# Optimization experiments

Measured on AMD Instinct MI355X. Metric: run time of the kernel, lower is better.

## Reference

```python
import jax, jax.numpy as jnp
import numpy as np

DIM = 512; HEADS = 8; DH = 64; INNER = HEADS * DH
GAMMA = 0.01; LREG = 1e-3
QB = 16; NS = 512


def _ln(x, g, b):
    mu = x.mean(-1, keepdims=True)
    var = jnp.var(x, axis=-1, keepdims=True)  # biased, matches torch LayerNorm
    return (x - mu) / jnp.sqrt(var + 1e-5) * g + b


def _std(x):
    return jnp.std(x, ddof=1)  # torch.std default is unbiased


def setup_inputs() -> dict:
    key = jax.random.key(0)
    ks = jax.random.split(key, 10)
    sc = lambda k, shape: (jax.random.normal(k, shape, jnp.float32) * 0.05)
    return {
        "q": jax.random.normal(ks[0], (QB, NS, DIM), jnp.float32),
        "k": jax.random.normal(ks[1], (QB, NS, DIM), jnp.float32),
        "v": jax.random.normal(ks[2], (QB, NS, DIM), jnp.float32),
        "ln1_g": jnp.ones((DIM,), jnp.float32),
        "ln1_b": jnp.zeros((DIM,), jnp.float32),
        "W_in": sc(ks[3], (DIM, INNER)),
        "wp_w1": sc(ks[4], (2 * DH, 2 * DH)),
        "wp_b1": jnp.zeros((2 * DH,), jnp.float32),
        "wp_ln_g": jnp.ones((2 * DH,), jnp.float32),
        "wp_ln_b": jnp.zeros((2 * DH,), jnp.float32),
        "wp_w2": sc(ks[5], (2 * DH, DH)),
        "wp_b2": jnp.zeros((DH,), jnp.float32),
        "wp_w3": sc(ks[6], (DH, 3)),
        "wp_b3": jnp.zeros((3,), jnp.float32),
        "weight_temp": jnp.array([0.5], jnp.float32),
        "W_out": sc(ks[7], (INNER, DIM)),
        "b_out": jnp.zeros((DIM,), jnp.float32),
    }


def _forward(q, k, v, ln1_g, ln1_b, W_in, wp_w1, wp_b1, wp_ln_g, wp_ln_b,
             wp_w2, wp_b2, wp_w3, wp_b3, weight_temp, W_out, b_out):
    eps = 1e-6

    def proj(t):  # LayerNorm -> Linear(no bias) -> [h, q, n, d]
        y = _ln(t, ln1_g, ln1_b) @ W_in
        Qb, Nb, _ = y.shape
        return y.reshape(Qb, Nb, HEADS, DH).transpose(2, 0, 1, 3)

    f_q, f_k, f_v = proj(q), proj(k), proj(v)
    m = f_k.shape[2]

    # --- cosine distance component ---
    dots_raw = jnp.einsum('hqnd,hqmd->hqnm', f_q, f_k)
    n1 = jnp.linalg.norm(f_q, axis=-1, keepdims=True) + eps          # [h,q,n,1]
    n2 = jnp.linalg.norm(f_k, axis=-1)[:, :, None, :] + eps          # [h,q,1,m]
    cosine_sim = jnp.clip(dots_raw / (n1 * n2), -0.9, 0.9)

    # --- regularized covariance component ---
    fkc = f_k - f_k.mean(axis=2, keepdims=True)   # center keys over n
    fqc = f_q - f_q.mean(axis=-1, keepdims=True)  # center queries over d
    cov = jnp.einsum('hqnd,hqmd->hqnm', fqc, fkc) / (DH ** 0.5 + 1e-6)
    cov = jnp.clip((LREG / max(m, 1)) * cov, -10.0, 10.0)

    # --- margin-based variance component (eval: adaptive_gamma = gamma) ---
    fqn = f_q / jnp.maximum(jnp.linalg.norm(f_q, axis=-1, keepdims=True), 1e-6)
    fkn = f_k / jnp.maximum(jnp.linalg.norm(f_k, axis=-1, keepdims=True), 1e-6)
    cs = jnp.clip(jnp.einsum('hqnd,hqmd->hqnm', fqn, fkn), -0.9, 0.9)
    margin = jnp.clip(GAMMA - cs, 0.0, 5.0)
    var_comp = jnp.broadcast_to(margin.mean(-1, keepdims=True), cs.shape)

    # --- dynamic per-head mixture weights ---
    feat = jnp.concatenate([f_q.mean((1, 2)), f_k.mean((1, 2))], axis=-1)  # [h, 2d]
    x = jax.nn.relu(_ln(feat @ wp_w1 + wp_b1, wp_ln_g, wp_ln_b))
    x = jax.nn.relu(x @ wp_w2 + wp_b2)
    wlog = jax.nn.softmax(x @ wp_w3 + wp_b3, axis=-1)  # predictor ends in Softmax
    wt = jnp.clip(weight_temp, 0.1, 2.0)
    w = jax.nn.softmax(wlog / wt, axis=-1)             # second softmax over temp
    w = jnp.clip(w, 0.05, 0.8)
    w = w / w.sum(-1, keepdims=True)
    cos_w = w[:, 0].reshape(HEADS, 1, 1, 1)
    cov_w = w[:, 1].reshape(HEADS, 1, 1, 1)
    var_w = w[:, 2].reshape(HEADS, 1, 1, 1)

    sg = jax.lax.stop_gradient  # norms are .detach()'d in torch
    dots = (cos_w * (cosine_sim / (sg(_std(cosine_sim)) + 1e-6))
            + cov_w * (cov / (sg(_std(cov)) + 1e-6) * 0.5)
            + var_w * (var_comp / (sg(_std(var_comp)) + 1e-6) * 0.5))

    ds = _std(dots)
    temp = jnp.where(ds < 1e-4, jnp.float32(0.1),
                     jnp.where(ds < 0.01, jnp.float32(0.3), 0.5 + ds))
    temp = jnp.clip(temp, 0.1, 3.0)

    attn = jax.nn.softmax(dots / temp, axis=-1)
    out = jnp.einsum('hqnm,hqmd->hqnd', attn, f_v)
    out = out.transpose(1, 2, 0, 3).reshape(q.shape[0], q.shape[1], INNER)
    return out @ W_out + b_out


def reference(q, k, v, ln1_g, ln1_b, W_in, wp_w1, wp_b1, wp_ln_g, wp_ln_b,
              wp_w2, wp_b2, wp_w3, wp_b3, weight_temp, W_out, b_out):
    return _forward(q, k, v, ln1_g, ln1_b, W_in, wp_w1, wp_b1, wp_ln_g,
                    wp_ln_b, wp_w2, wp_b2, wp_w3, wp_b3, weight_temp,
                    W_out, b_out)
```

## Files before the change

kernel.cpp:

```cpp
#include <hip/hip_runtime.h>
#include <math.h>

#define H 8
#define NS 512
#define D 64

typedef __bf16 bf16x8 __attribute__((ext_vector_type(8)));
typedef float f32x4 __attribute__((ext_vector_type(4)));
typedef short s16x8 __attribute__((ext_vector_type(8)));
typedef short s16x4 __attribute__((ext_vector_type(4)));

#define CS2 ((1e-3f/512.f)/(8.f+1e-6f))

static __device__ __forceinline__ f32x4 mfma16(bf16x8 a, bf16x8 b, f32x4 c){
  return __builtin_amdgcn_mfma_f32_16x16x32_bf16(a,b,c,0,0,0);
}
static __device__ __forceinline__ float b2f(unsigned short s){
  union { unsigned u; float f; } v; v.u = ((unsigned)s)<<16; return v.f;
}
static __device__ __forceinline__ unsigned short f2b(float f){
  union { float f; unsigned u; } v; v.f = f;
  unsigned r = v.u + 0x7FFFu + ((v.u>>16)&1u);
  return (unsigned short)(r>>16);
}
static __device__ __forceinline__ float wred64(float v){
  #pragma unroll
  for(int m=32; m>0; m>>=1) v += __shfl_xor(v, m, 64);
  return v;
}

constexpr size_t OFF_XNB = 0;
constexpr size_t OFF_FQB = 6291456;
constexpr size_t OFF_FKB = 8388608;
constexpr size_t OFF_FVB = 10485760;
constexpr size_t OFF_FVT = 12582912;
constexpr size_t OFF_WT  = 14680064;
constexpr size_t OFF_WOH = 14811136;
constexpr size_t OFF_WOL = 14942208;
constexpr size_t OFF_OHH = 15073280;
constexpr size_t OFF_OHL = 17170432;
constexpr size_t OFF_ARR = 19267584;
constexpr size_t OFF_MKB = OFF_ARR + 9*65536;
constexpr size_t OFF_SMK = OFF_MKB + 8192;
constexpr size_t OFF_COEF= OFF_SMK + 128;
constexpr size_t OFF_DBL = OFF_COEF + 32;
constexpr size_t NDBL    = 72 + 1024;

__global__ __launch_bounds__(256) void k_tw(const float* __restrict__ W, unsigned short* __restrict__ WT,
    double* __restrict__ dbl){
  int bx = blockIdx.x; int kt = bx>>3, nt = bx&7;
  int t = threadIdx.x;
  if(bx==0){
    for(int i=t;i<(int)NDBL;i+=256) dbl[i]=0.0;
  }
  __shared__ float tile[64][65];
  #pragma unroll
  for(int i=0;i<4;i++){
    int row = (t>>4) + i*16; int col = (t&15)*4;
    float4 v = *(const float4*)(W + (size_t)(kt*64+row)*512 + nt*64 + col);
    tile[row][col]=v.x; tile[row][col+1]=v.y; tile[row][col+2]=v.z; tile[row][col+3]=v.w;
  }
  __syncthreads();
  #pragma unroll
  for(int i=0;i<4;i++){
    int n = (t>>4) + i*16; int ck = (t&15)*4;
    s16x4 o;
    #pragma unroll
    for(int j=0;j<4;j++) o[j] = (short)f2b(tile[ck+j][n]);
    *(s16x4*)(WT + (size_t)(nt*64+n)*512 + kt*64 + ck) = o;
  }
}

__global__ __launch_bounds__(256) void k_two(const float* __restrict__ W,
    unsigned short* __restrict__ WTh, unsigned short* __restrict__ WTl){
  int bx = blockIdx.x; int kt = bx>>3, nt = bx&7;
  __shared__ float tile[64][65];
  int t = threadIdx.x;
  #pragma unroll
  for(int i=0;i<4;i++){
    int row = (t>>4) + i*16; int col = (t&15)*4;
    float4 v = *(const float4*)(W + (size_t)(kt*64+row)*512 + nt*64 + col);
    tile[row][col]=v.x; tile[row][col+1]=v.y; tile[row][col+2]=v.z; tile[row][col+3]=v.w;
  }
  __syncthreads();
  #pragma unroll
  for(int i=0;i<4;i++){
    int n = (t>>4) + i*16; int ck = (t&15)*4;
    s16x4 oh_, ol_;
    #pragma unroll
    for(int j=0;j<4;j++){
      float x = tile[ck+j][n];
      unsigned short hi = f2b(x);
      oh_[j] = (short)hi;
      ol_[j] = (short)f2b(x - b2f(hi));
    }
    *(s16x4*)(WTh + (size_t)(nt*64+n)*512 + kt*64 + ck) = oh_;
    *(s16x4*)(WTl + (size_t)(nt*64+n)*512 + kt*64 + ck) = ol_;
  }
}

__global__ __launch_bounds__(256) void k_ln(const float* __restrict__ q,
    const float* __restrict__ k, const float* __restrict__ v,
    const float* __restrict__ g, const float* __restrict__ b,
    unsigned short* __restrict__ xnb){
  int row = blockIdx.x*4 + (threadIdx.x>>6); int t = threadIdx.x & 63;
  const float* src = (row < 8192) ? q : ((row < 16384) ? k : v);
  int r = row & 8191;
  const float4* sp = (const float4*)(src + (size_t)r*512);
  float4 v1 = sp[t*2], v2 = sp[t*2+1];
  float s  = v1.x+v1.y+v1.z+v1.w + v2.x+v2.y+v2.z+v2.w;
  float ss = v1.x*v1.x+v1.y*v1.y+v1.z*v1.z+v1.w*v1.w
           + v2.x*v2.x+v2.y*v2.y+v2.z*v2.z+v2.w*v2.w;
  s = wred64(s); ss = wred64(ss);
  float mu = s*(1.f/512.f);
  float var = ss*(1.f/512.f) - mu*mu;
  float rstd = rsqrtf(var + 1e-5f);
  const float4* gp = (const float4*)g; const float4* bp = (const float4*)b;
  float4 g1 = gp[t*2], g2 = gp[t*2+1], b1 = bp[t*2], b2 = bp[t*2+1];
  s16x8 o;
  o[0]=(short)f2b((v1.x-mu)*rstd*g1.x+b1.x); o[1]=(short)f2b((v1.y-mu)*rstd*g1.y+b1.y);
  o[2]=(short)f2b((v1.z-mu)*rstd*g1.z+b1.z); o[3]=(short)f2b((v1.w-mu)*rstd*g1.w+b1.w);
  o[4]=(short)f2b((v2.x-mu)*rstd*g2.x+b2.x); o[5]=(short)f2b((v2.y-mu)*rstd*g2.y+b2.y);
  o[6]=(short)f2b((v2.z-mu)*rstd*g2.z+b2.z); o[7]=(short)f2b((v2.w-mu)*rstd*g2.w+b2.w);
  *(s16x8*)(xnb + (size_t)row*512 + t*8) = o;
}

__global__ __launch_bounds__(256) void k_mm1(const unsigned short* __restrict__ xnb,
    const unsigned short* __restrict__ WT,
    unsigned short* __restrict__ fqb, unsigned short* __restrict__ fkb,
    unsigned short* __restrict__ fvb){
  __shared__ __align__(16) unsigned short As[128*64];
  __shared__ __align__(16) unsigned short Bs[128*64];
  int t = threadIdx.x; int w = t>>6; int l = t&63; int g = l>>4, lc = l&15;
  int Rb = blockIdx.x*128, cb = blockIdx.y*128;
  int wr = (w>>1)*64, wc = (w&1)*64;
  f32x4 acc[4][4];
  #pragma unroll
  for(int i=0;i<4;i++)
    #pragma unroll
    for(int j=0;j<4;j++) acc[i][j] = (f32x4){0.f,0.f,0.f,0.f};
  for(int k0=0; k0<512; k0+=64){
    __syncthreads();
    #pragma unroll
    for(int i=0;i<4;i++){
      int c = t + i*256; int row = c>>3, k8 = c&7;
      s16x8 va = *(const s16x8*)(xnb + (size_t)(Rb+row)*512 + k0 + k8*8);
      *(s16x8*)((char*)As + row*128 + ((k8*16) ^ ((row&7)<<4))) = va;
      s16x8 vb = *(const s16x8*)(WT + (size_t)(cb+row)*512 + k0 + k8*8);
      *(s16x8*)((char*)Bs + row*128 + ((k8*16) ^ ((row&7)<<4))) = vb;
    }
    __syncthreads();
    #pragma unroll
    for(int ks=0; ks<2; ks++){
      bf16x8 ar[4], br[4];
      #pragma unroll
      for(int rt=0; rt<4; rt++){
        int row = wr + rt*16 + lc;
        ar[rt] = *(const bf16x8*)((const char*)As + row*128 + (((ks*4+g)*16) ^ ((row&7)<<4)));
      }
      #pragma unroll
      for(int ct=0; ct<4; ct++){
        int row = wc + ct*16 + lc;
        br[ct] = *(const bf16x8*)((const char*)Bs + row*128 + (((ks*4+g)*16) ^ ((row&7)<<4)));
      }
      #pragma unroll
      for(int rt=0; rt<4; rt++)
        #pragma unroll
        for(int ct=0; ct<4; ct++)
          acc[rt][ct] = mfma16(ar[rt], br[ct], acc[rt][ct]);
    }
  }
  #pragma unroll
  for(int rt=0; rt<4; rt++){
    #pragma unroll
    for(int r=0; r<4; r++){
      int R = Rb + wr + rt*16 + g*4 + r;
      int tsel = R>>13; int rr = R&8191;
      unsigned short* dst = (tsel==0)?fqb:((tsel==1)?fkb:fvb);
      #pragma unroll
      for(int ct=0; ct<4; ct++){
        int c = cb + wc + ct*16 + lc;
        dst[(size_t)rr*512 + c] = f2b(acc[rt][ct][r]);
      }
    }
  }
}

__global__ __launch_bounds__(1024) void k_colstats(const unsigned short* __restrict__ fqb,
    const unsigned short* __restrict__ fkb,
    float* __restrict__ mkb, float* __restrict__ smk, double* featd){
  int hq = blockIdx.x; int h = hq>>4, q = hq&15;
  int t = threadIdx.x; int d = t&63; int g = t>>6;
  __shared__ float cq[16][64], ck[16][64];
  float aq=0.f, ak=0.f;
  for(int n=g; n<512; n+=16){
    size_t base = (size_t)(q*512+n)*512 + h*64 + d;
    aq += b2f(fqb[base]);
    ak += b2f(fkb[base]);
  }
  cq[g][d]=aq; ck[g][d]=ak;
  __syncthreads();
  if(t<64){
    float sq=0.f, sk2=0.f;
    #pragma unroll
    for(int i=0;i<16;i++){ sq+=cq[i][t]; sk2+=ck[i][t]; }
    atomicAdd(&featd[h*128+t], (double)sq);
    atomicAdd(&featd[h*128+64+t], (double)sk2);
    float mk = sk2*(1.f/512.f);
    mkb[hq*64+t]=mk;
    cq[0][t]=mk;
  }
  __syncthreads();
  if(t<64){
    float s = wred64(cq[0][t]);
    if(t==0) smk[hq]=s;
  }
}

__global__ __launch_bounds__(256) void k_rowstats(const unsigned short* __restrict__ fqb,
    const unsigned short* __restrict__ fkb, const float* __restrict__ mkb,
    float* __restrict__ ri1, float* __restrict__ mq,
    float* __restrict__ qdm, float* __restrict__ ri2,
    float* __restrict__ sk){
  int b = blockIdx.x; int hq = b>>1; int h = hq>>4, q = hq&15;
  int n = (b&1)*256 + threadIdx.x;
  __shared__ float mk[64];
  if(threadIdx.x<64) mk[threadIdx.x] = mkb[hq*64+threadIdx.x];
  __syncthreads();
  const unsigned short* fr = fqb + (size_t)(q*512+n)*512 + h*64;
  const unsigned short* kr = fkb + (size_t)(q*512+n)*512 + h*64;
  float sq=0.f, ssq=0.f, dq=0.f, sks=0.f, ssk=0.f;
  #pragma unroll
  for(int j=0;j<8;j++){
    s16x8 vq = *(const s16x8*)(fr + j*8);
    s16x8 vk = *(const s16x8*)(kr + j*8);
    #pragma unroll
    for(int e=0;e<8;e++){
      float a = b2f((unsigned short)vq[e]);
      float c = b2f((unsigned short)vk[e]);
      sq += a; ssq += a*a; dq += a*mk[j*8+e];
      sks += c; ssk += c*c;
    }
  }
  int idx = hq*512 + n;
  float nq = sqrtf(ssq);
  ri1[idx]  = 1.f/(nq+1e-6f);
  mq[idx]   = sq*(1.f/64.f);
  qdm[idx]  = dq;
  float nk = sqrtf(ssk);
  ri2[idx]  = 1.f/(nk+1e-6f);
  sk[idx]   = sks;
}

__global__ __launch_bounds__(256) void k_vt(const unsigned short* __restrict__ fvb,
    unsigned short* __restrict__ fvT){
  int bx = blockIdx.x; int hq = bx>>2, nc = bx&3;
  int h = hq>>4, q = hq&15; int n0 = nc*128;
  __shared__ float tile[128][65];
  int t = threadIdx.x;
  #pragma unroll
  for(int i=0;i<4;i++){
    int c = t + i*256; int row = c>>3, k8 = c&7;
    s16x8 v = *(const s16x8*)(fvb + (size_t)(q*512 + n0 + row)*512 + h*64 + k8*8);
    #pragma unroll
    for(int j=0;j<8;j++) tile[row][k8*8+j] = b2f((unsigned short)v[j]);
  }
  __syncthreads();
  #pragma unroll
  for(int i=0;i<4;i++){
    int c = t + i*256; int d = c>>4, n8 = c&15;
    s16x8 o;
    #pragma unroll
    for(int j=0;j<8;j++) o[j] = (short)f2b(tile[n8*8+j][d]);
    *(s16x8*)(fvT + (size_t)(hq*64 + d)*512 + n0 + n8*8) = o;
  }
}

__global__ __launch_bounds__(256) void k_comp(const unsigned short* __restrict__ fqb,
    const unsigned short* __restrict__ fkb,
    const float* __restrict__ ri1,
    const float* __restrict__ mq, const float* __restrict__ qdm,
    const float* __restrict__ ri2,
    const float* __restrict__ sk, const float* __restrict__ smk,
    float* __restrict__ mxcg, float* __restrict__ mxvg, double* headsum){
  int bx = blockIdx.x; int hq = bx>>3; int rt = bx&7;
  int h = hq>>4, q = hq&15; int n0 = rt*64;
  __shared__ __align__(16) unsigned short Qs[64*64];
  __shared__ __align__(16) unsigned short Ks[128*64];
  __shared__ float ri2f[512], skf[512];
  __shared__ float red[4][9];
  int t = threadIdx.x; int w = t>>6; int l = t&63; int g = l>>4, lc = l&15;
  for(int i=t; i<512; i+=256){
    ri2f[i]=ri2[hq*NS+i]; skf[i]=sk[hq*NS+i];
  }
  #pragma unroll
  for(int i=0;i<2;i++){
    int c = t + i*256; int row = c>>3, k8 = c&7;
    s16x8 v = *(const s16x8*)(fqb + (size_t)(q*512 + n0 + row)*512 + h*64 + k8*8);
    *(s16x8*)((char*)Qs + row*128 + ((k8*16) ^ ((row&7)<<4))) = v;
  }
  float ri1r[4], mqr[4], qdmr[4];
  #pragma unroll
  for(int r=0;r<4;r++){
    int n = hq*NS + n0 + w*16 + g*4 + r;
    ri1r[r]=ri1[n]; mqr[r]=mq[n]; qdmr[r]=qdm[n];
  }
  float smkv = smk[hq];
  __syncthreads();
  bf16x8 aq[2];
  #pragma unroll
  for(int ks=0;ks<2;ks++){
    int row = 16*w + lc;
    aq[ks] = *(const bf16x8*)((const char*)Qs + row*128 + (((ks*4+g)*16) ^ ((row&7)<<4)));
  }
  float p0=0,p1=0,p2=0,p3=0,p4=0;
  float rm_m[4]={0,0,0,0}, rm_c[4]={0,0,0,0}, rm_v[4]={0,0,0,0};
  float mxc[4]={-1e30f,-1e30f,-1e30f,-1e30f}, mxv[4]={-1e30f,-1e30f,-1e30f,-1e30f};
  for(int mc=0; mc<4; mc++){
    __syncthreads();
    #pragma unroll
    for(int i=0;i<4;i++){
      int c = t + i*256; int row = c>>3, k8 = c&7;
      s16x8 v = *(const s16x8*)(fkb + (size_t)(q*512 + mc*128 + row)*512 + h*64 + k8*8);
      *(s16x8*)((char*)Ks + row*128 + ((k8*16) ^ ((row&7)<<4))) = v;
    }
    __syncthreads();
    #pragma unroll 2
    for(int mt=0; mt<8; mt++){
      f32x4 dacc = (f32x4){0.f,0.f,0.f,0.f};
      #pragma unroll
      for(int ks=0;ks<2;ks++){
        int row = mt*16 + lc;
        bf16x8 bk = *(const bf16x8*)((const char*)Ks + row*128 + (((ks*4+g)*16) ^ ((row&7)<<4)));
        dacc = mfma16(aq[ks], bk, dacc);
      }
      int m = mc*128 + mt*16 + lc;
      float r2 = ri2f[m], skc = skf[m];
      #pragma unroll
      for(int r=0;r<4;r++){
        float dv = dacc[r];
        float cosv = fminf(fmaxf(dv*ri1r[r]*r2, -0.9f), 0.9f);
        float inner = dv - qdmr[r] - mqr[r]*skc + mqr[r]*smkv;
        float covv = fminf(fmaxf(CS2*inner, -10.f), 10.f);
        float marg = fmaxf(0.01f - cosv, 0.f);
        p0 += cosv; p1 += cosv*cosv; p2 += covv; p3 += covv*covv; p4 += cosv*covv;
        rm_m[r]+=marg; rm_c[r]+=cosv; rm_v[r]+=covv;
        mxc[r]=fmaxf(mxc[r],cosv); mxv[r]=fmaxf(mxv[r],covv);
      }
    }
  }
  #pragma unroll
  for(int off=1; off<16; off<<=1){
    #pragma unroll
    for(int r=0;r<4;r++){
      rm_m[r]+=__shfl_xor(rm_m[r],off,64);
      rm_c[r]+=__shfl_xor(rm_c[r],off,64);
      rm_v[r]+=__shfl_xor(rm_v[r],off,64);
      mxc[r]=fmaxf(mxc[r],__shfl_xor(mxc[r],off,64));
      mxv[r]=fmaxf(mxv[r],__shfl_xor(mxv[r],off,64));
    }
  }
  float q0=0,q1=0,q2=0,q3=0;
  if(lc==0){
    #pragma unroll
    for(int r=0;r<4;r++){
      float vmv = rm_m[r]*(1.f/512.f);
      q0+=vmv; q1+=vmv*vmv; q2+=vmv*rm_c[r]; q3+=vmv*rm_v[r];
      int n = n0 + w*16 + g*4 + r;
      mxcg[hq*NS+n]=mxc[r]; mxvg[hq*NS+n]=mxv[r];
    }
  }
  float all9[9] = {p0,p1,p2,p3,p4,q0,q1,q2,q3};
  #pragma unroll
  for(int j=0;j<9;j++){
    float vv = wred64(all9[j]);
    if(l==0) red[w][j]=vv;
  }
  __syncthreads();
  if(t<9){
    double s = (double)red[0][t]+(double)red[1][t]+(double)red[2][t]+(double)red[3][t];
    atomicAdd(&headsum[h*9+t], s);
  }
}

__global__ __launch_bounds__(1024) void k_finalize(const double* headsum, const double* featd,
    const float* __restrict__ w1, const float* __restrict__ b1,
    const float* __restrict__ lng, const float* __restrict__ lnb,
    const float* __restrict__ w2, const float* __restrict__ b2,
    const float* __restrict__ w3, const float* __restrict__ b3,
    const float* __restrict__ wtemp, float* coef){
  __shared__ float featS[8][128];
  __shared__ float x1S[8][128];
  __shared__ float x2S[8][64];
  __shared__ float redS[8][4];
  __shared__ float oS[8][3];
  __shared__ float whS[8][3];
  int t = threadIdx.x;
  int h = t>>7, j = t&127;
  featS[h][j] = (float)(featd[t] * (1.0/8192.0));
  __syncthreads();
  float a = 0.f;
  #pragma unroll 16
  for(int i=0;i<128;i++) a += featS[h][i]*w1[(size_t)i*128+j];
  a += b1[j];
  {
    float s = a, ss = a*a;
    #pragma unroll
    for(int m=32;m>0;m>>=1){ s += __shfl_xor(s,m,64); ss += __shfl_xor(ss,m,64); }
    int wv = (t>>6)&1;
    if((t&63)==0){ redS[h][wv*2]=s; redS[h][wv*2+1]=ss; }
  }
  __syncthreads();
  {
    float sum = redS[h][0]+redS[h][2], sumsq = redS[h][1]+redS[h][3];
    float mu = sum*(1.f/128.f);
    float var = sumsq*(1.f/128.f)-mu*mu;
    float rstd = rsqrtf(var+1e-5f);
    x1S[h][j] = fmaxf((a-mu)*rstd*lng[j]+lnb[j], 0.f);
  }
  __syncthreads();
  if(t < 512){
    int h2 = t>>6, j2 = t&63;
    float s2 = 0.f;
    #pragma unroll 16
    for(int i=0;i<128;i++) s2 += x1S[h2][i]*w2[(size_t)i*64+j2];
    x2S[h2][j2] = fmaxf(s2+b2[j2], 0.f);
  }
  __syncthreads();
  if(t < 24){
    int h3 = t/3, j3 = t-h3*3;
    float s3=0.f;
    #pragma unroll 16
    for(int i=0;i<64;i++) s3 += x2S[h3][i]*w3[i*3+j3];
    oS[h3][j3] = s3 + b3[j3];
  }
  __syncthreads();
  if(t < 8){
    float o0=oS[t][0], o1=oS[t][1], o2=oS[t][2];
    float mx=fmaxf(o0,fmaxf(o1,o2));
    float e0=expf(o0-mx), e1=expf(o1-mx), e2=expf(o2-mx), se=e0+e1+e2;
    float l0=e0/se, l1=e1/se, l2=e2/se;
    float wt=fminf(fmaxf(wtemp[0],0.1f),2.0f);
    l0/=wt; l1/=wt; l2/=wt;
    mx=fmaxf(l0,fmaxf(l1,l2));
    e0=expf(l0-mx); e1=expf(l1-mx); e2=expf(l2-mx); se=e0+e1+e2;
    float u0=fminf(fmaxf(e0/se,0.05f),0.8f);
    float u1=fminf(fmaxf(e1/se,0.05f),0.8f);
    float u2=fminf(fmaxf(e2/se,0.05f),0.8f);
    float su=u0+u1+u2;
    whS[t][0]=u0/su; whS[t][1]=u1/su; whS[t][2]=u2/su;
  }
  __syncthreads();
  if(t==0){
    const double N = 33554432.0;
    double gs[9];
    for(int jj=0;jj<9;jj++){ double s=0; for(int hh=0;hh<8;hh++) s+=headsum[hh*9+jj]; gs[jj]=s; }
    auto sd = [&](double s, double ss)->double{
      double v=(ss - s*s/N)/(N-1.0); return v>0.0 ? sqrt(v) : 0.0;
    };
    double std_cos = sd(gs[0],gs[1]);
    double std_cov = sd(gs[2],gs[3]);
    double std_vm  = sd(512.0*gs[5], 512.0*gs[6]);
    double sdot=0.0, sdot2=0.0;
    double Af[8], Bf[8];
    for(int hh=0;hh<8;hh++){
      const double* hs = headsum + hh*9;
      double A = (double)whS[hh][0]/(std_cos+1e-6);
      double B = (double)whS[hh][1]/(std_cov+1e-6)*0.5;
      double C = (double)whS[hh][2]/(std_vm +1e-6)*0.5;
      sdot  += A*hs[0] + B*hs[2] + C*512.0*hs[5];
      sdot2 += A*A*hs[1] + B*B*hs[3] + C*C*512.0*hs[6]
             + 2.0*A*B*hs[4] + 2.0*A*C*hs[7] + 2.0*B*C*hs[8];
      Af[hh]=A; Bf[hh]=B;
    }
    double dstd = sd(sdot, sdot2);
    double temp = dstd < 1e-4 ? 0.1 : (dstd < 0.01 ? 0.3 : 0.5 + dstd);
    temp = fmin(fmax(temp, 0.1), 3.0);
    for(int hh=0;hh<8;hh++){
      coef[hh]   = (float)(Af[hh]/temp);
      coef[8+hh] = (float)(Bf[hh]/temp);
    }
    coef[16] = (float)temp;
  }
}

__global__ __launch_bounds__(256) void k_flash(const unsigned short* __restrict__ fqb,
    const unsigned short* __restrict__ fkb, const unsigned short* __restrict__ fvT,
    const float* __restrict__ ri1, const float* __restrict__ mq,
    const float* __restrict__ qdm, const float* __restrict__ ri2,
    const float* __restrict__ sk, const float* __restrict__ smk,
    const float* __restrict__ mxcg, const float* __restrict__ mxvg,
    const float* __restrict__ coef,
    unsigned short* __restrict__ ohh, unsigned short* __restrict__ ohl){
  int bx = blockIdx.x; int hq = bx>>3; int rt = bx&7;
  int h = hq>>4, q = hq&15; int n0 = rt*64;
  __shared__ __align__(16) unsigned short Qs[64*64];
  __shared__ __align__(16) unsigned short Ks[128*64];
  __shared__ __align__(16) unsigned short Vt[64*128];
  __shared__ __align__(16) unsigned short Ps[4][16*40];
  __shared__ float ri2f[512], skf[512];
  int t = threadIdx.x; int w = t>>6; int l = t&63; int g = l>>4, lc = l&15;
  for(int i=t; i<512; i+=256){ ri2f[i]=ri2[hq*NS+i]; skf[i]=sk[hq*NS+i]; }
  #pragma unroll
  for(int i=0;i<2;i++){
    int c = t + i*256; int row = c>>3, k8 = c&7;
    s16x8 v = *(const s16x8*)(fqb + (size_t)(q*512 + n0 + row)*512 + h*64 + k8*8);
    *(s16x8*)((char*)Qs + row*128 + ((k8*16) ^ ((row&7)<<4))) = v;
  }
  float Ah = coef[h], Bh = coef[8+h];
  float ri1r[4], mqr[4], qdmr[4], Mr[4];
  #pragma unroll
  for(int r=0;r<4;r++){
    int n = hq*NS + n0 + w*16 + g*4 + r;
    ri1r[r]=ri1[n]; mqr[r]=mq[n]; qdmr[r]=qdm[n];
    Mr[r] = Ah*mxcg[n] + Bh*mxvg[n];
  }
  float smkv = smk[hq];
  __syncthreads();
  bf16x8 aq[2];
  #pragma unroll
  for(int ks=0;ks<2;ks++){
    int row = 16*w + lc;
    aq[ks] = *(const bf16x8*)((const char*)Qs + row*128 + (((ks*4+g)*16) ^ ((row&7)<<4)));
  }
  f32x4 acc[4];
  #pragma unroll
  for(int dt=0;dt<4;dt++) acc[dt] = (f32x4){0.f,0.f,0.f,0.f};
  float lsum[4]={0.f,0.f,0.f,0.f};
  unsigned short* Pw = &Ps[w][0];
  for(int mc=0; mc<4; mc++){
    __syncthreads();
    #pragma unroll
    for(int i=0;i<4;i++){
      int c = t + i*256; int row = c>>3, k8 = c&7;
      s16x8 v = *(const s16x8*)(fkb + (size_t)(q*512 + mc*128 + row)*512 + h*64 + k8*8);
      *(s16x8*)((char*)Ks + row*128 + ((k8*16) ^ ((row&7)<<4))) = v;
    }
    #pragma unroll
    for(int i=0;i<4;i++){
      int c = t + i*256; int d = c>>4, m8 = c&15;
      s16x8 v = *(const s16x8*)(fvT + (size_t)(hq*64 + d)*512 + mc*128 + m8*8);
      *(s16x8*)((char*)Vt + d*256 + ((m8*16) ^ ((d&7)<<4))) = v;
    }
    __syncthreads();
    #pragma unroll 1
    for(int mt2=0; mt2<4; mt2++){
      #pragma unroll
      for(int half=0; half<2; half++){
        int mt = mt2*2 + half;
        f32x4 dacc = (f32x4){0.f,0.f,0.f,0.f};
        #pragma unroll
        for(int ks=0;ks<2;ks++){
          int row = mt*16 + lc;
          bf16x8 bk = *(const bf16x8*)((const char*)Ks + row*128 + (((ks*4+g)*16) ^ ((row&7)<<4)));
          dacc = mfma16(aq[ks], bk, dacc);
        }
        int m = mc*128 + mt*16 + lc;
        float r2 = ri2f[m], skc = skf[m];
        #pragma unroll
        for(int r=0;r<4;r++){
          float dv = dacc[r];
          float cosv = fminf(fmaxf(dv*ri1r[r]*r2, -0.9f), 0.9f);
          float inner = dv - qdmr[r] - mqr[r]*skc + mqr[r]*smkv;
          float covv = fminf(fmaxf(CS2*inner, -10.f), 10.f);
          float sv = Ah*cosv + Bh*covv;
          float pe = __expf(fmaxf(sv - Mr[r], -60.f));
          lsum[r] += pe;
          Pw[(g*4+r)*40 + lc + half*16] = f2b(pe);
        }
      }
      asm volatile("s_waitcnt lgkmcnt(0)" ::: "memory");
      bf16x8 ap = *(const bf16x8*)((const char*)Pw + lc*80 + g*16);
      #pragma unroll
      for(int dt=0;dt<4;dt++){
        int drow = dt*16 + lc;
        bf16x8 bv = *(const bf16x8*)((const char*)Vt + drow*256 + (((mt2*4+g)*16) ^ ((drow&7)<<4)));
        acc[dt] = mfma16(ap, bv, acc[dt]);
      }
    }
  }
  #pragma unroll
  for(int off=1; off<16; off<<=1){
    #pragma unroll
    for(int r=0;r<4;r++) lsum[r] += __shfl_xor(lsum[r], off, 64);
  }
  #pragma unroll
  for(int r=0;r<4;r++){
    float inv = 1.f/lsum[r];
    int n = n0 + w*16 + g*4 + r;
    #pragma unroll
    for(int dt=0;dt<4;dt++){
      size_t idx = (size_t)(q*512 + n)*512 + h*64 + dt*16 + lc;
      float val = acc[dt][r]*inv;
      unsigned short hi = f2b(val);
      ohh[idx] = hi;
      ohl[idx] = f2b(val - b2f(hi));
    }
  }
}

__global__ __launch_bounds__(256) void k_gout2(const unsigned short* __restrict__ Ahp,
    const unsigned short* __restrict__ Alp,
    const unsigned short* __restrict__ Bhp, const unsigned short* __restrict__ Blp,
    const float* __restrict__ bias, float* __restrict__ Cout){
  __shared__ __align__(16) unsigned short AsH[128*64];
  __shared__ __align__(16) unsigned short AsL[128*64];
  __shared__ __align__(16) unsigned short BsH[128*64];
  __shared__ __align__(16) unsigned short BsL[128*64];
  int t = threadIdx.x; int w = t>>6; int l = t&63; int g = l>>4, lc = l&15;
  int Rb = blockIdx.x*128, cb = blockIdx.y*128;
  int wr = (w>>1)*64, wc = (w&1)*64;
  f32x4 acc[4][4];
  #pragma unroll
  for(int i=0;i<4;i++)
    #pragma unroll
    for(int j=0;j<4;j++) acc[i][j] = (f32x4){0.f,0.f,0.f,0.f};
  for(int k0=0; k0<512; k0+=64){
    __syncthreads();
    #pragma unroll
    for(int i=0;i<4;i++){
      int c = t + i*256; int row = c>>3, k8 = c&7;
      int sw = (k8*16) ^ ((row&7)<<4);
      *(s16x8*)((char*)AsH + row*128 + sw) = *(const s16x8*)(Ahp + (size_t)(Rb+row)*512 + k0 + k8*8);
      *(s16x8*)((char*)AsL + row*128 + sw) = *(const s16x8*)(Alp + (size_t)(Rb+row)*512 + k0 + k8*8);
      *(s16x8*)((char*)BsH + row*128 + sw) = *(const s16x8*)(Bhp + (size_t)(cb+row)*512 + k0 + k8*8);
      *(s16x8*)((char*)BsL + row*128 + sw) = *(const s16x8*)(Blp + (size_t)(cb+row)*512 + k0 + k8*8);
    }
    __syncthreads();
    #pragma unroll
    for(int ks=0; ks<2; ks++){
      bf16x8 arh[4], arl[4], brh[4], brl[4];
      #pragma unroll
      for(int rt=0; rt<4; rt++){
        int row = wr + rt*16 + lc;
        int off = row*128 + (((ks*4+g)*16) ^ ((row&7)<<4));
        arh[rt] = *(const bf16x8*)((const char*)AsH + off);
        arl[rt] = *(const bf16x8*)((const char*)AsL + off);
      }
      #pragma unroll
      for(int ct=0; ct<4; ct++){
        int row = wc + ct*16 + lc;
        int off = row*128 + (((ks*4+g)*16) ^ ((row&7)<<4));
        brh[ct] = *(const bf16x8*)((const char*)BsH + off);
        brl[ct] = *(const bf16x8*)((const char*)BsL + off);
      }
      #pragma unroll
      for(int rt=0; rt<4; rt++)
        #pragma unroll
        for(int ct=0; ct<4; ct++){
          acc[rt][ct] = mfma16(arh[rt], brh[ct], acc[rt][ct]);
          acc[rt][ct] = mfma16(arh[rt], brl[ct], acc[rt][ct]);
          acc[rt][ct] = mfma16(arl[rt], brh[ct], acc[rt][ct]);
        }
    }
  }
  #pragma unroll
  for(int rt=0; rt<4; rt++){
    #pragma unroll
    for(int r=0; r<4; r++){
      int R = Rb + wr + rt*16 + g*4 + r;
      #pragma unroll
      for(int ct=0; ct<4; ct++){
        int c = cb + wc + ct*16 + lc;
        Cout[(size_t)R*512 + c] = acc[rt][ct][r] + bias[c];
      }
    }
  }
}

extern "C" void kernel_launch(void* const* d_in, const int* in_sizes, int n_in,
                              void* d_out, int out_size, void* d_ws, size_t ws_size,
                              hipStream_t stream){
  const float* q    = (const float*)d_in[0];
  const float* k    = (const float*)d_in[1];
  const float* v    = (const float*)d_in[2];
  const float* ln1g = (const float*)d_in[3];
  const float* ln1b = (const float*)d_in[4];
  const float* Win  = (const float*)d_in[5];
  const float* w1   = (const float*)d_in[6];
  const float* b1   = (const float*)d_in[7];
  const float* lng  = (const float*)d_in[8];
  const float* lnb  = (const float*)d_in[9];
  const float* w2   = (const float*)d_in[10];
  const float* b2   = (const float*)d_in[11];
  const float* w3   = (const float*)d_in[12];
  const float* b3   = (const float*)d_in[13];
  const float* wtemp= (const float*)d_in[14];
  const float* Wout = (const float*)d_in[15];
  const float* bout = (const float*)d_in[16];

  float* w = (float*)d_ws;
  unsigned short* xnb = (unsigned short*)(w + OFF_XNB);
  unsigned short* fqb = (unsigned short*)(w + OFF_FQB);
  unsigned short* fkb = (unsigned short*)(w + OFF_FKB);
  unsigned short* fvb = (unsigned short*)(w + OFF_FVB);
  unsigned short* fvT = (unsigned short*)(w + OFF_FVT);
  unsigned short* wtb = (unsigned short*)(w + OFF_WT);
  unsigned short* woh = (unsigned short*)(w + OFF_WOH);
  unsigned short* wol = (unsigned short*)(w + OFF_WOL);
  unsigned short* ohh = (unsigned short*)(w + OFF_OHH);
  unsigned short* ohl = (unsigned short*)(w + OFF_OHL);
  float* ri1  = w + OFF_ARR + 0*65536;
  float* mq_  = w + OFF_ARR + 2*65536;
  float* qdm  = w + OFF_ARR + 3*65536;
  float* ri2  = w + OFF_ARR + 4*65536;
  float* sk_  = w + OFF_ARR + 6*65536;
  float* mxc  = w + OFF_ARR + 7*65536;
  float* mxv  = w + OFF_ARR + 8*65536;
  float* mkb  = w + OFF_MKB;
  float* smk_ = w + OFF_SMK;
  float* coef = w + OFF_COEF;
  double* dbl = (double*)(w + OFF_DBL);
  double* headsum = dbl;
  double* featd   = dbl + 72;

  k_tw<<<64, 256, 0, stream>>>(Win, wtb, dbl);
  k_two<<<64, 256, 0, stream>>>(Wout, woh, wol);
  k_ln<<<6144, 256, 0, stream>>>(q, k, v, ln1g, ln1b, xnb);
  k_mm1<<<dim3(192,4), 256, 0, stream>>>(xnb, wtb, fqb, fkb, fvb);
  k_colstats<<<128, 1024, 0, stream>>>(fqb, fkb, mkb, smk_, featd);
  k_rowstats<<<256, 256, 0, stream>>>(fqb, fkb, mkb, ri1, mq_, qdm, ri2, sk_);
  k_vt<<<512, 256, 0, stream>>>(fvb, fvT);
  k_comp<<<1024, 256, 0, stream>>>(fqb, fkb, ri1, mq_, qdm, ri2, sk_, smk_, mxc, mxv, headsum);
  k_finalize<<<1, 1024, 0, stream>>>(headsum, featd, w1, b1, lng, lnb, w2, b2, w3, b3, wtemp, coef);
  k_flash<<<1024, 256, 0, stream>>>(fqb, fkb, fvT, ri1, mq_, qdm, ri2, sk_, smk_, mxc, mxv, coef, ohh, ohl);
  k_gout2<<<dim3(64,4), 256, 0, stream>>>(ohh, ohl, woh, wol, bout, (float*)d_out);
}
```

Baseline: 174.3 us.

## Fold smk into sk, drop cov clamp/scale, use exp2 and packed P stores

New measurement: 168.6 us. -3.3%, faster.

```diff
diff --git a/kernel.cpp b/kernel.cpp
--- a/kernel.cpp
+++ b/kernel.cpp
@@ -11,6 +11,7 @@
 typedef short s16x4 __attribute__((ext_vector_type(4)));
 
 #define CS2 ((1e-3f/512.f)/(8.f+1e-6f))
+#define LOG2E 1.4426950408889634
 
 static __device__ __forceinline__ f32x4 mfma16(bf16x8 a, bf16x8 b, f32x4 c){
   return __builtin_amdgcn_mfma_f32_16x16x32_bf16(a,b,c,0,0,0);
@@ -219,6 +220,7 @@
 
 __global__ __launch_bounds__(256) void k_rowstats(const unsigned short* __restrict__ fqb,
     const unsigned short* __restrict__ fkb, const float* __restrict__ mkb,
+    const float* __restrict__ smk,
     float* __restrict__ ri1, float* __restrict__ mq,
     float* __restrict__ qdm, float* __restrict__ ri2,
     float* __restrict__ sk){
@@ -227,6 +229,7 @@
   __shared__ float mk[64];
   if(threadIdx.x<64) mk[threadIdx.x] = mkb[hq*64+threadIdx.x];
   __syncthreads();
+  float smkv = smk[hq];
   const unsigned short* fr = fqb + (size_t)(q*512+n)*512 + h*64;
   const unsigned short* kr = fkb + (size_t)(q*512+n)*512 + h*64;
   float sq=0.f, ssq=0.f, dq=0.f, sks=0.f, ssk=0.f;
@@ -249,7 +252,7 @@
   qdm[idx]  = dq;
   float nk = sqrtf(ssk);
   ri2[idx]  = 1.f/(nk+1e-6f);
-  sk[idx]   = sks;
+  sk[idx]   = sks - smkv;
 }
 
 __global__ __launch_bounds__(256) void k_vt(const unsigned short* __restrict__ fvb,
@@ -271,7 +274,12 @@
     int c = t + i*256; int d = c>>4, n8 = c&15;
     s16x8 o;
     #pragma unroll
-    for(int j=0;j<8;j++) o[j] = (short)f2b(tile[n8*8+j][d]);
+    for(int j=0;j<8;j++){
+      int p = n8*8+j;
+      int pl = p & 31;
+      int src = (p & ~31) | (16*(pl&1) + (pl>>1));
+      o[j] = (short)f2b(tile[src][d]);
+    }
     *(s16x8*)(fvT + (size_t)(hq*64 + d)*512 + n0 + n8*8) = o;
   }
 }
@@ -281,7 +289,7 @@
     const float* __restrict__ ri1,
     const float* __restrict__ mq, const float* __restrict__ qdm,
     const float* __restrict__ ri2,
-    const float* __restrict__ sk, const float* __restrict__ smk,
+    const float* __restrict__ skp,
     float* __restrict__ mxcg, float* __restrict__ mxvg, double* headsum){
   int bx = blockIdx.x; int hq = bx>>3; int rt = bx&7;
   int h = hq>>4, q = hq&15; int n0 = rt*64;
@@ -291,7 +299,7 @@
   __shared__ float red[4][9];
   int t = threadIdx.x; int w = t>>6; int l = t&63; int g = l>>4, lc = l&15;
   for(int i=t; i<512; i+=256){
-    ri2f[i]=ri2[hq*NS+i]; skf[i]=sk[hq*NS+i];
+    ri2f[i]=ri2[hq*NS+i]; skf[i]=skp[hq*NS+i];
   }
   #pragma unroll
   for(int i=0;i<2;i++){
@@ -305,7 +313,6 @@
     int n = hq*NS + n0 + w*16 + g*4 + r;
     ri1r[r]=ri1[n]; mqr[r]=mq[n]; qdmr[r]=qdm[n];
   }
-  float smkv = smk[hq];
   __syncthreads();
   bf16x8 aq[2];
   #pragma unroll
@@ -313,7 +320,7 @@
     int row = 16*w + lc;
     aq[ks] = *(const bf16x8*)((const char*)Qs + row*128 + (((ks*4+g)*16) ^ ((row&7)<<4)));
   }
-  float p0=0,p1=0,p2=0,p3=0,p4=0;
+  float p1=0,p3=0,p4=0;
   float rm_m[4]={0,0,0,0}, rm_c[4]={0,0,0,0}, rm_v[4]={0,0,0,0};
   float mxc[4]={-1e30f,-1e30f,-1e30f,-1e30f}, mxv[4]={-1e30f,-1e30f,-1e30f,-1e30f};
   for(int mc=0; mc<4; mc++){
@@ -335,20 +342,21 @@
         dacc = mfma16(aq[ks], bk, dacc);
       }
       int m = mc*128 + mt*16 + lc;
-      float r2 = ri2f[m], skc = skf[m];
+      float r2 = ri2f[m], sc = skf[m];
       #pragma unroll
       for(int r=0;r<4;r++){
         float dv = dacc[r];
         float cosv = fminf(fmaxf(dv*ri1r[r]*r2, -0.9f), 0.9f);
-        float inner = dv - qdmr[r] - mqr[r]*skc + mqr[r]*smkv;
-        float covv = fminf(fmaxf(CS2*inner, -10.f), 10.f);
+        float inner = (dv - qdmr[r]) - mqr[r]*sc;
         float marg = fmaxf(0.01f - cosv, 0.f);
-        p0 += cosv; p1 += cosv*cosv; p2 += covv; p3 += covv*covv; p4 += cosv*covv;
-        rm_m[r]+=marg; rm_c[r]+=cosv; rm_v[r]+=covv;
-        mxc[r]=fmaxf(mxc[r],cosv); mxv[r]=fmaxf(mxv[r],covv);
-      }
-    }
-  }
+        p1 += cosv*cosv; p3 += inner*inner; p4 += cosv*inner;
+        rm_m[r]+=marg; rm_c[r]+=cosv; rm_v[r]+=inner;
+        mxc[r]=fmaxf(mxc[r],cosv); mxv[r]=fmaxf(mxv[r],inner);
+      }
+    }
+  }
+  float p0 = rm_c[0]+rm_c[1]+rm_c[2]+rm_c[3];
+  float p2 = rm_v[0]+rm_v[1]+rm_v[2]+rm_v[3];
   #pragma unroll
   for(int off=1; off<16; off<<=1){
     #pragma unroll
@@ -453,32 +461,33 @@
   __syncthreads();
   if(t==0){
     const double N = 33554432.0;
+    const double CS2d = (double)CS2;
     double gs[9];
     for(int jj=0;jj<9;jj++){ double s=0; for(int hh=0;hh<8;hh++) s+=headsum[hh*9+jj]; gs[jj]=s; }
     auto sd = [&](double s, double ss)->double{
       double v=(ss - s*s/N)/(N-1.0); return v>0.0 ? sqrt(v) : 0.0;
     };
     double std_cos = sd(gs[0],gs[1]);
-    double std_cov = sd(gs[2],gs[3]);
+    double std_cov = sd(CS2d*gs[2], CS2d*CS2d*gs[3]);
     double std_vm  = sd(512.0*gs[5], 512.0*gs[6]);
     double sdot=0.0, sdot2=0.0;
     double Af[8], Bf[8];
     for(int hh=0;hh<8;hh++){
       const double* hs = headsum + hh*9;
       double A = (double)whS[hh][0]/(std_cos+1e-6);
-      double B = (double)whS[hh][1]/(std_cov+1e-6)*0.5;
+      double Bi = (double)whS[hh][1]/(std_cov+1e-6)*0.5*CS2d;
       double C = (double)whS[hh][2]/(std_vm +1e-6)*0.5;
-      sdot  += A*hs[0] + B*hs[2] + C*512.0*hs[5];
-      sdot2 += A*A*hs[1] + B*B*hs[3] + C*C*512.0*hs[6]
-             + 2.0*A*B*hs[4] + 2.0*A*C*hs[7] + 2.0*B*C*hs[8];
-      Af[hh]=A; Bf[hh]=B;
+      sdot  += A*hs[0] + Bi*hs[2] + C*512.0*hs[5];
+      sdot2 += A*A*hs[1] + Bi*Bi*hs[3] + C*C*512.0*hs[6]
+             + 2.0*A*Bi*hs[4] + 2.0*A*C*hs[7] + 2.0*Bi*C*hs[8];
+      Af[hh]=A; Bf[hh]=Bi;
     }
     double dstd = sd(sdot, sdot2);
     double temp = dstd < 1e-4 ? 0.1 : (dstd < 0.01 ? 0.3 : 0.5 + dstd);
     temp = fmin(fmax(temp, 0.1), 3.0);
     for(int hh=0;hh<8;hh++){
-      coef[hh]   = (float)(Af[hh]/temp);
-      coef[8+hh] = (float)(Bf[hh]/temp);
+      coef[hh]   = (float)(Af[hh]/temp*LOG2E);
+      coef[8+hh] = (float)(Bf[hh]/temp*LOG2E);
     }
     coef[16] = (float)temp;
   }
@@ -488,7 +497,7 @@
     const unsigned short* __restrict__ fkb, const unsigned short* __restrict__ fvT,
     const float* __restrict__ ri1, const float* __restrict__ mq,
     const float* __restrict__ qdm, const float* __restrict__ ri2,
-    const float* __restrict__ sk, const float* __restrict__ smk,
+    const float* __restrict__ skp,
     const float* __restrict__ mxcg, const float* __restrict__ mxvg,
     const float* __restrict__ coef,
     unsigned short* __restrict__ ohh, unsigned short* __restrict__ ohl){
@@ -500,7 +509,7 @@
   __shared__ __align__(16) unsigned short Ps[4][16*40];
   __shared__ float ri2f[512], skf[512];
   int t = threadIdx.x; int w = t>>6; int l = t&63; int g = l>>4, lc = l&15;
-  for(int i=t; i<512; i+=256){ ri2f[i]=ri2[hq*NS+i]; skf[i]=sk[hq*NS+i]; }
+  for(int i=t; i<512; i+=256){ ri2f[i]=ri2[hq*NS+i]; skf[i]=skp[hq*NS+i]; }
   #pragma unroll
   for(int i=0;i<2;i++){
     int c = t + i*256; int row = c>>3, k8 = c&7;
@@ -515,7 +524,6 @@
     ri1r[r]=ri1[n]; mqr[r]=mq[n]; qdmr[r]=qdm[n];
     Mr[r] = Ah*mxcg[n] + Bh*mxvg[n];
   }
-  float smkv = smk[hq];
   __syncthreads();
   bf16x8 aq[2];
   #pragma unroll
@@ -528,6 +536,7 @@
   for(int dt=0;dt<4;dt++) acc[dt] = (f32x4){0.f,0.f,0.f,0.f};
   float lsum[4]={0.f,0.f,0.f,0.f};
   unsigned short* Pw = &Ps[w][0];
+  unsigned* Pu = (unsigned*)Pw;
   for(int mc=0; mc<4; mc++){
     __syncthreads();
     #pragma unroll
@@ -545,29 +554,32 @@
     __syncthreads();
     #pragma unroll 1
     for(int mt2=0; mt2<4; mt2++){
-      #pragma unroll
-      for(int half=0; half<2; half++){
-        int mt = mt2*2 + half;
-        f32x4 dacc = (f32x4){0.f,0.f,0.f,0.f};
-        #pragma unroll
-        for(int ks=0;ks<2;ks++){
-          int row = mt*16 + lc;
-          bf16x8 bk = *(const bf16x8*)((const char*)Ks + row*128 + (((ks*4+g)*16) ^ ((row&7)<<4)));
-          dacc = mfma16(aq[ks], bk, dacc);
-        }
-        int m = mc*128 + mt*16 + lc;
-        float r2 = ri2f[m], skc = skf[m];
-        #pragma unroll
-        for(int r=0;r<4;r++){
-          float dv = dacc[r];
-          float cosv = fminf(fmaxf(dv*ri1r[r]*r2, -0.9f), 0.9f);
-          float inner = dv - qdmr[r] - mqr[r]*skc + mqr[r]*smkv;
-          float covv = fminf(fmaxf(CS2*inner, -10.f), 10.f);
-          float sv = Ah*cosv + Bh*covv;
-          float pe = __expf(fmaxf(sv - Mr[r], -60.f));
-          lsum[r] += pe;
-          Pw[(g*4+r)*40 + lc + half*16] = f2b(pe);
-        }
+      f32x4 d0 = (f32x4){0.f,0.f,0.f,0.f};
+      f32x4 d1 = (f32x4){0.f,0.f,0.f,0.f};
+      #pragma unroll
+      for(int ks=0;ks<2;ks++){
+        int row0 = (mt2*2)*16 + lc;
+        bf16x8 bk0 = *(const bf16x8*)((const char*)Ks + row0*128 + (((ks*4+g)*16) ^ ((row0&7)<<4)));
+        d0 = mfma16(aq[ks], bk0, d0);
+        int row1 = (mt2*2+1)*16 + lc;
+        bf16x8 bk1 = *(const bf16x8*)((const char*)Ks + row1*128 + (((ks*4+g)*16) ^ ((row1&7)<<4)));
+        d1 = mfma16(aq[ks], bk1, d1);
+      }
+      int m0 = mc*128 + mt2*32 + lc;
+      float r20 = ri2f[m0],    sc0 = skf[m0];
+      float r21 = ri2f[m0+16], sc1 = skf[m0+16];
+      #pragma unroll
+      for(int r=0;r<4;r++){
+        float dv0 = d0[r], dv1 = d1[r];
+        float c0 = fminf(fmaxf(dv0*ri1r[r]*r20, -0.9f), 0.9f);
+        float c1 = fminf(fmaxf(dv1*ri1r[r]*r21, -0.9f), 0.9f);
+        float i0 = (dv0 - qdmr[r]) - mqr[r]*sc0;
+        float i1 = (dv1 - qdmr[r]) - mqr[r]*sc1;
+        float pe0 = __builtin_amdgcn_exp2f(fmaxf(Ah*c0 + Bh*i0 - Mr[r], -120.f));
+        float pe1 = __builtin_amdgcn_exp2f(fmaxf(Ah*c1 + Bh*i1 - Mr[r], -120.f));
+        lsum[r] += pe0 + pe1;
+        unsigned pk = ((unsigned)f2b(pe1) << 16) | (unsigned)f2b(pe0);
+        Pu[(g*4+r)*20 + lc] = pk;
       }
       asm volatile("s_waitcnt lgkmcnt(0)" ::: "memory");
       bf16x8 ap = *(const bf16x8*)((const char*)Pw + lc*80 + g*16);
@@ -719,10 +731,10 @@
   k_ln<<<6144, 256, 0, stream>>>(q, k, v, ln1g, ln1b, xnb);
   k_mm1<<<dim3(192,4), 256, 0, stream>>>(xnb, wtb, fqb, fkb, fvb);
   k_colstats<<<128, 1024, 0, stream>>>(fqb, fkb, mkb, smk_, featd);
-  k_rowstats<<<256, 256, 0, stream>>>(fqb, fkb, mkb, ri1, mq_, qdm, ri2, sk_);
+  k_rowstats<<<256, 256, 0, stream>>>(fqb, fkb, mkb, smk_, ri1, mq_, qdm, ri2, sk_);
   k_vt<<<512, 256, 0, stream>>>(fvb, fvT);
-  k_comp<<<1024, 256, 0, stream>>>(fqb, fkb, ri1, mq_, qdm, ri2, sk_, smk_, mxc, mxv, headsum);
+  k_comp<<<1024, 256, 0, stream>>>(fqb, fkb, ri1, mq_, qdm, ri2, sk_, mxc, mxv, headsum);
   k_finalize<<<1, 1024, 0, stream>>>(headsum, featd, w1, b1, lng, lnb, w2, b2, w3, b3, wtemp, coef);
-  k_flash<<<1024, 256, 0, stream>>>(fqb, fkb, fvT, ri1, mq_, qdm, ri2, sk_, smk_, mxc, mxv, coef, ohh, ohl);
+  k_flash<<<1024, 256, 0, stream>>>(fqb, fkb, fvT, ri1, mq_, qdm, ri2, sk_, mxc, mxv, coef, ohh, ohl);
   k_gout2<<<dim3(64,4), 256, 0, stream>>>(ohh, ohl, woh, wol, bout, (float*)d_out);
 }
```
